# Performance work log

Measured on AMD Instinct MI355X. Metric: run time of the kernel, lower is better.

## Reference

```python
import jax, jax.numpy as jnp
import numpy as np

N_NODES = 100000

def _gcn_layer(h, src, dst, norm, W, b, n_nodes):
    # GCNConv: x @ W, then symmetric-normalized scatter-add over edges (incl. self-loops)
    h = h @ W                                  # [N, F_out]
    msg = h[src] * norm[:, None]               # [E_tot, F_out]
    out = jax.ops.segment_sum(msg, dst, num_segments=n_nodes)
    return out + b


def setup_inputs() -> dict:
    key = jax.random.key(0)
    k1, k2, k3, k4 = jax.random.split(key, 4)
    N, E, F_in, H, C = N_NODES, 3200000, 128, 16, 16
    x = jax.random.normal(k1, (N, F_in), dtype=jnp.float32)
    edge_index = jax.random.randint(k2, (2, E), 0, N, dtype=jnp.int64)
    W1 = jax.random.normal(k3, (F_in, H), dtype=jnp.float32) * (1.0 / np.sqrt(F_in))
    b1 = jnp.zeros((H,), dtype=jnp.float32)
    W2 = jax.random.normal(k4, (H, C), dtype=jnp.float32) * (1.0 / np.sqrt(H))
    b2 = jnp.zeros((C,), dtype=jnp.float32)
    return {"x": x, "edge_index": edge_index, "W1": W1, "b1": b1, "W2": W2, "b2": b2}


def reference(x, edge_index, W1, b1, W2, b2):
    N = x.shape[0]
    loops = jnp.arange(N, dtype=edge_index.dtype)
    src = jnp.concatenate([edge_index[0], loops])  # messages flow src -> dst (PyG convention)
    dst = jnp.concatenate([edge_index[1], loops])
    # symmetric normalization: deg^{-1/2}[src] * deg^{-1/2}[dst], deg counted on dst w/ self-loops
    deg = jnp.zeros((N,), dtype=x.dtype).at[dst].add(1.0)
    dinv = jax.lax.rsqrt(jnp.where(deg > 0, deg, 1.0))
    norm = dinv[src] * dinv[dst]                   # [E_tot]

    h = _gcn_layer(x, src, dst, norm, W1, b1, N)
    h = jax.nn.relu(h)
    # F.dropout(training=self.training): eval mode -> identity (deterministic reference)
    h = _gcn_layer(h, src, dst, norm, W2, b2, N)
    return jax.nn.log_softmax(h, axis=1)
```

## Files before the change

kernel.cpp:

```cpp
#include <hip/hip_runtime.h>
#include <hip/hip_bf16.h>
#include <math.h>


#define F_IN 128
#define H 16
#define NPB 128
#define MAX_NB 800
#define NBLK 256
#define BINT 1024
#define SMAX 4864
#define PFD 3

typedef __hip_bfloat16 bf16;

__device__ __forceinline__ float bflo(unsigned v) { return __uint_as_float(v << 16); }
__device__ __forceinline__ float bfhi(unsigned v) { return __uint_as_float(v & 0xffff0000u); }

__device__ __forceinline__ int swz(int p) { return (p & 7) * 32 + (p >> 3); }

__global__ void histA_kernel(const int* __restrict__ dst, int* __restrict__ hist_t,
                             int E, int NB) {
    __shared__ int h[MAX_NB];
    int b = swz(blockIdx.x);
    long long e0 = (long long)E * b / NBLK;
    long long e1 = (long long)E * (b + 1) / NBLK;
    for (int i = threadIdx.x; i < NB; i += BINT) h[i] = 0;
    __syncthreads();
    for (long long e = e0 + threadIdx.x; e < e1; e += BINT)
        atomicAdd(&h[dst[e] >> 7], 1);
    __syncthreads();
    for (int i = threadIdx.x; i < NB; i += BINT) hist_t[i * NBLK + b] = h[i];
}

__global__ void colscan_kernel(int* __restrict__ hist_t, int* __restrict__ btot) {
    __shared__ int s[NBLK];
    int j = blockIdx.x;
    int t = threadIdx.x;
    int v = hist_t[j * NBLK + t];
    s[t] = v;
    __syncthreads();
    for (int off = 1; off < NBLK; off <<= 1) {
        int w = (t >= off) ? s[t - off] : 0;
        __syncthreads();
        s[t] += w;
        __syncthreads();
    }
    hist_t[j * NBLK + t] = s[t] - v;
    if (t == NBLK - 1) btot[j] = s[t];
}

__global__ void bucketscan_kernel(const int* __restrict__ btot, int* __restrict__ base, int NB) {
    __shared__ int s[1024];
    int t = threadIdx.x;
    s[t] = (t < NB) ? btot[t] : 0;
    __syncthreads();
    for (int off = 1; off < 1024; off <<= 1) {
        int v = (t >= off) ? s[t - off] : 0;
        __syncthreads();
        s[t] += v;
        __syncthreads();
    }
    if (t < NB) base[t] = s[t] - btot[t];
    if (t == NB - 1) base[NB] = s[t];
}

__global__ void binC_kernel(const int* __restrict__ src, const int* __restrict__ dst,
                            const int* __restrict__ hist_t, const int* __restrict__ base,
                            unsigned* __restrict__ packed, int E, int NB) {
    __shared__ int pos[MAX_NB];
    int b = swz(blockIdx.x);
    long long e0 = (long long)E * b / NBLK;
    long long e1 = (long long)E * (b + 1) / NBLK;
    for (int i = threadIdx.x; i < NB; i += BINT)
        pos[i] = base[i] + hist_t[i * NBLK + b];
    __syncthreads();
    for (long long e = e0 + threadIdx.x; e < e1; e += BINT) {
        int d = dst[e];
        int bk = d >> 7;
        int p = atomicAdd(&pos[bk], 1);
        packed[p] = (unsigned)src[e] | ((unsigned)(d & 127) << 17);
    }
}

__global__ void sortcsr_kernel(const unsigned* __restrict__ packed, const int* __restrict__ base,
                               unsigned* __restrict__ sorted, int* __restrict__ rowptr,
                               float* __restrict__ dinv, int N, int E) {
    __shared__ unsigned ssort[SMAX];
    __shared__ int cnt[NPB], offs[NPB], cur[NPB];
    int b = blockIdx.x;
    int e0 = base[b];
    int len = base[b + 1] - e0;
    if (len > SMAX) len = SMAX;
    int T = blockDim.x;

    for (int i = threadIdx.x; i < NPB; i += T) cnt[i] = 0;
    __syncthreads();
    for (int i = threadIdx.x; i < len; i += T)
        atomicAdd(&cnt[packed[e0 + i] >> 17], 1);
    __syncthreads();
    if (threadIdx.x < NPB) offs[threadIdx.x] = cnt[threadIdx.x];
    __syncthreads();
    for (int off = 1; off < NPB; off <<= 1) {
        int v = 0;
        if (threadIdx.x < NPB && threadIdx.x >= off) v = offs[threadIdx.x - off];
        __syncthreads();
        if (threadIdx.x < NPB) offs[threadIdx.x] += v;
        __syncthreads();
    }
    if (threadIdx.x < NPB) {
        int ex = offs[threadIdx.x] - cnt[threadIdx.x];
        cur[threadIdx.x] = ex;
        int node = b * NPB + threadIdx.x;
        if (node < N) {
            rowptr[node] = e0 + ex;
            dinv[node] = rsqrtf(1.0f + (float)cnt[threadIdx.x]);
        }
    }
    __syncthreads();
    for (int i = threadIdx.x; i < len; i += T) {
        unsigned p = packed[e0 + i];
        int pos = atomicAdd(&cur[p >> 17], 1);
        ssort[pos] = p;
    }
    __syncthreads();
    for (int i = threadIdx.x; i < len; i += T) sorted[e0 + i] = ssort[i];
    if (b == 0 && threadIdx.x == 0) rowptr[N] = E;
}

#define XPAD 132
__global__ void xw1_kernel(const float* __restrict__ x, const float* __restrict__ W1,
                           const float* __restrict__ dinv, bf16* __restrict__ u, int n) {
    __shared__ float sW1[F_IN * H];
    __shared__ float sx[16 * XPAD];
    for (int t = threadIdx.x; t < F_IN * H; t += blockDim.x) sW1[t] = W1[t];

    int basei = blockIdx.x * 16;
    for (int idx = threadIdx.x; idx < 512; idx += 256) {
        int r = idx >> 5;
        int kk = (idx & 31) << 2;
        int row = basei + r;
        float4 v = make_float4(0.f, 0.f, 0.f, 0.f);
        if (row < n) v = *(const float4*)(x + (size_t)row * F_IN + kk);
        *(float4*)(sx + r * XPAD + kk) = v;
    }
    __syncthreads();

    int r = threadIdx.x >> 4;
    int j = threadIdx.x & 15;
    int row = basei + r;
    if (row >= n) return;

    const float* xr = sx + r * XPAD;
    float acc = 0.0f;
#pragma unroll 16
    for (int k = 0; k < F_IN; k++) acc += xr[k] * sW1[k * H + j];
    u[(size_t)row * H + j] = __float2bfloat16(dinv[row] * acc);
}

#define GATHER_TILE(UVPTR)                                                      \
    int lane = threadIdx.x & 63;                                                \
    int wave = threadIdx.x >> 6;                                                \
    int j4 = lane & 3, g = lane >> 2;                                           \
    int nodeBase = blockIdx.x * 64 + wave * 16;                                 \
    int r0c = 0, r1c = 0;                                                       \
    unsigned svc[PFD]; uint2 uvc[PFD];                                          \
    {   int node = nodeBase;                                                    \
        if (node < N) { r0c = rowptr[node]; r1c = rowptr[node + 1]; }           \
        _Pragma("unroll")                                                       \
        for (int m = 0; m < PFD; m++) {                                         \
            int k = r0c + g + 16 * m;                                           \
            if (k < r1c) svc[m] = sorted[k];                                    \
        }                                                                       \
        _Pragma("unroll")                                                       \
        for (int m = 0; m < PFD; m++) {                                         \
            int k = r0c + g + 16 * m;                                           \
            if (k < r1c) uvc[m] = UVPTR[(size_t)(svc[m] & 0x1FFFF) * 4 + j4];   \
        }                                                                       \
    }                                                                           \
    for (int t = 0; t < 16; t++) {                                              \
        int r0n = 0, r1n = 0;                                                   \
        unsigned svn[PFD];                                                      \
        if (t < 15) {                                                           \
            int nn = nodeBase + t + 1;                                          \
            if (nn < N) { r0n = rowptr[nn]; r1n = rowptr[nn + 1]; }             \
            _Pragma("unroll")                                                   \
            for (int m = 0; m < PFD; m++) {                                     \
                int k = r0n + g + 16 * m;                                       \
                if (k < r1n) svn[m] = sorted[k];                                \
            }                                                                   \
        }                                                                       \
        float ax = 0.f, ay = 0.f, az = 0.f, aw = 0.f;                           \
        _Pragma("unroll")                                                       \
        for (int m = 0; m < PFD; m++) {                                         \
            int k = r0c + g + 16 * m;                                           \
            if (k < r1c) {                                                      \
                ax += bflo(uvc[m].x); ay += bfhi(uvc[m].x);                     \
                az += bflo(uvc[m].y); aw += bfhi(uvc[m].y);                     \
            }                                                                   \
        }                                                                       \
        for (int k = r0c + g + 16 * PFD; k < r1c; k += 16) {                    \
            uint2 va = UVPTR[(size_t)(sorted[k] & 0x1FFFF) * 4 + j4];           \
            ax += bflo(va.x); ay += bfhi(va.x);                                 \
            az += bflo(va.y); aw += bfhi(va.y);                                 \
        }                                                                       \
        ax += __shfl_xor(ax, 4);  ay += __shfl_xor(ay, 4);                      \
        az += __shfl_xor(az, 4);  aw += __shfl_xor(aw, 4);                      \
        ax += __shfl_xor(ax, 8);  ay += __shfl_xor(ay, 8);                      \
        az += __shfl_xor(az, 8);  aw += __shfl_xor(aw, 8);                      \
        ax += __shfl_xor(ax, 16); ay += __shfl_xor(ay, 16);                     \
        az += __shfl_xor(az, 16); aw += __shfl_xor(aw, 16);                     \
        ax += __shfl_xor(ax, 32); ay += __shfl_xor(ay, 32);                     \
        az += __shfl_xor(az, 32); aw += __shfl_xor(aw, 32);                     \
        if (g == 0) {                                                           \
            float* tp = &tile[(wave * 16 + t) * 16 + 4 * j4];                   \
            tp[0] = ax; tp[1] = ay; tp[2] = az; tp[3] = aw;                     \
        }                                                                       \
        if (t < 15) {                                                           \
            r0c = r0n; r1c = r1n;                                               \
            _Pragma("unroll")                                                   \
            for (int m = 0; m < PFD; m++) {                                     \
                int k = r0n + g + 16 * m;                                       \
                svc[m] = svn[m];                                                \
                if (k < r1n) uvc[m] = UVPTR[(size_t)(svn[m] & 0x1FFFF) * 4 + j4]; \
            }                                                                   \
        }                                                                       \
    }

__global__ void gatherfin1_kernel(const unsigned* __restrict__ sorted, const int* __restrict__ rowptr,
                                  const bf16* __restrict__ u, const float* __restrict__ dinv,
                                  const float* __restrict__ b1, const float* __restrict__ W2,
                                  bf16* __restrict__ u2, int N) {
    __shared__ float tile[64 * 16];
    __shared__ float sW2[256];
    __shared__ float sb1[16];
    sW2[threadIdx.x] = W2[threadIdx.x];
    if (threadIdx.x < 16) sb1[threadIdx.x] = b1[threadIdx.x];

    const uint2* uvp = (const uint2*)u;
    GATHER_TILE(uvp)
    __syncthreads();

    int jj = threadIdx.x & 15;
    for (int rr = 0; rr < 4; rr++) {
        int rl = (threadIdx.x >> 4) + rr * 16;
        int node = blockIdx.x * 64 + rl;
        float h = 0.f, di = 0.f;
        if (node < N) {
            di = dinv[node];
            h = di * (tile[rl * 16 + jj] + __bfloat162float(u[(size_t)node * H + jj])) + sb1[jj];
            h = fmaxf(h, 0.f);
        }
        float acc2 = 0.f;
#pragma unroll
        for (int kk = 0; kk < 16; kk++) {
            float hk = __shfl(h, kk, 16);
            acc2 += hk * sW2[kk * 16 + jj];
        }
        if (node < N) u2[(size_t)node * H + jj] = __float2bfloat16(di * acc2);
    }
}

__global__ void gatherfin2_kernel(const unsigned* __restrict__ sorted, const int* __restrict__ rowptr,
                                  const bf16* __restrict__ u2, const float* __restrict__ dinv,
                                  const float* __restrict__ b2, float* __restrict__ out, int N) {
    __shared__ float tile[64 * 16];
    __shared__ float sb2[16];
    if (threadIdx.x < 16) sb2[threadIdx.x] = b2[threadIdx.x];

    const uint2* uvp = (const uint2*)u2;
    GATHER_TILE(uvp)
    __syncthreads();

    int jj = threadIdx.x & 15;
    for (int rr = 0; rr < 4; rr++) {
        int rl = (threadIdx.x >> 4) + rr * 16;
        int node = blockIdx.x * 64 + rl;
        if (node >= N) continue;
        float di = dinv[node];
        float v = di * (tile[rl * 16 + jj] + __bfloat162float(u2[(size_t)node * H + jj])) + sb2[jj];

        float m = v;
#pragma unroll
        for (int off = 8; off >= 1; off >>= 1) m = fmaxf(m, __shfl_xor(m, off, 16));
        float ex = __expf(v - m);
        float s = ex;
#pragma unroll
        for (int off = 8; off >= 1; off >>= 1) s += __shfl_xor(s, off, 16);

        out[(size_t)node * H + jj] = v - m - __logf(s);
    }
}

extern "C" void kernel_launch(void* const* d_in, const int* in_sizes, int n_in,
                              void* d_out, int out_size, void* d_ws, size_t ws_size,
                              hipStream_t stream) {
    const float* x = (const float*)d_in[0];
    const int* edge_index = (const int*)d_in[1];
    const float* W1 = (const float*)d_in[2];
    const float* b1 = (const float*)d_in[3];
    const float* W2 = (const float*)d_in[4];
    const float* b2 = (const float*)d_in[5];
    float* out = (float*)d_out;

    const int N = in_sizes[0] / F_IN;
    const int E = in_sizes[1] / 2;
    const int* src = edge_index;
    const int* dst = edge_index + E;
    const int NB = (N + NPB - 1) / NPB;

    float* dinv = (float*)d_ws;
    bf16* u = (bf16*)(dinv + N);
    bf16* u2 = (bf16*)((unsigned*)u + (size_t)N * H / 2);
    unsigned* packed = (unsigned*)((unsigned*)u2 + (size_t)N * H / 2);
    unsigned* sorted = packed + E;
    int* hist_t = (int*)(sorted + E);
    int* rowptr = hist_t + (size_t)MAX_NB * NBLK;
    int* btot = rowptr + N + 1;
    int* base = btot + NB;

    histA_kernel<<<NBLK, BINT, 0, stream>>>(dst, hist_t, E, NB);
    colscan_kernel<<<NB, NBLK, 0, stream>>>(hist_t, btot);
    bucketscan_kernel<<<1, 1024, 0, stream>>>(btot, base, NB);
    binC_kernel<<<NBLK, BINT, 0, stream>>>(src, dst, hist_t, base, packed, E, NB);
    sortcsr_kernel<<<NB, 512, 0, stream>>>(packed, base, sorted, rowptr, dinv, N, E);

    xw1_kernel<<<(N + 15) / 16, 256, 0, stream>>>(x, W1, dinv, u, N);
    gatherfin1_kernel<<<(N + 63) / 64, 256, 0, stream>>>(sorted, rowptr, u, dinv, b1, W2, u2, N);
    gatherfin2_kernel<<<(N + 63) / 64, 256, 0, stream>>>(sorted, rowptr, u2, dinv, b2, out, N);
}
```

Measured before the change: 234.6 us.

## Deepen gather prefetch pipeline and broadcast row pointers via wave shuffles

Each wave loads the 16 rowptr pairs once, one per lane, and hands them out with __shfl instead of reloading them for every node. The gather loop becomes a fully unrolled two-stage software pipeline: edge indices are prefetched two nodes ahead and feature rows one node ahead, using double-buffered registers. The aim is to hide more global-memory latency in the irregular gather, at the cost of more registers and possibly lower occupancy.

New measurement: 248.8 us. 1.06x slower.

```diff
diff --git a/kernel.cpp b/kernel.cpp
--- a/kernel.cpp
+++ b/kernel.cpp
@@ -163,43 +163,60 @@
     int wave = threadIdx.x >> 6;                                                \
     int j4 = lane & 3, g = lane >> 2;                                           \
     int nodeBase = blockIdx.x * 64 + wave * 16;                                 \
-    int r0c = 0, r1c = 0;                                                       \
-    unsigned svc[PFD]; uint2 uvc[PFD];                                          \
-    {   int node = nodeBase;                                                    \
-        if (node < N) { r0c = rowptr[node]; r1c = rowptr[node + 1]; }           \
+    int rA = 0, rB = 0;                                                         \
+    {   int nl = nodeBase + lane;                                               \
+        if (lane < 16 && nl < N) { rA = rowptr[nl]; rB = rowptr[nl + 1]; }      \
+    }                                                                           \
+    unsigned sv[2][PFD]; uint2 uv[2][PFD];                                      \
+    {                               \
+        int p00 = __shfl(rA, 0), p01 = __shfl(rB, 0);                           \
+        int p10 = __shfl(rA, 1), p11 = __shfl(rB, 1);                           \
         _Pragma("unroll")                                                       \
         for (int m = 0; m < PFD; m++) {                                         \
-            int k = r0c + g + 16 * m;                                           \
-            if (k < r1c) svc[m] = sorted[k];                                    \
+            int k = p00 + g + 16 * m;                                           \
+            if (k < p01) sv[0][m] = sorted[k];                                  \
         }                                                                       \
         _Pragma("unroll")                                                       \
         for (int m = 0; m < PFD; m++) {                                         \
-            int k = r0c + g + 16 * m;                                           \
-            if (k < r1c) uvc[m] = UVPTR[(size_t)(svc[m] & 0x1FFFF) * 4 + j4];   \
+            int k = p10 + g + 16 * m;                                           \
+            if (k < p11) sv[1][m] = sorted[k];                                  \
+        }                                                                       \
+        _Pragma("unroll")                                                       \
+        for (int m = 0; m < PFD; m++) {                                         \
+            int k = p00 + g + 16 * m;                                           \
+            if (k < p01) uv[0][m] = UVPTR[(size_t)(sv[0][m] & 0x1FFFF) * 4 + j4]; \
         }                                                                       \
     }                                                                           \
+    _Pragma("unroll")                                                           \
     for (int t = 0; t < 16; t++) {                                              \
-        int r0n = 0, r1n = 0;                                                   \
-        unsigned svn[PFD];                                                      \
-        if (t < 15) {                                                           \
-            int nn = nodeBase + t + 1;                                          \
-            if (nn < N) { r0n = rowptr[nn]; r1n = rowptr[nn + 1]; }             \
+        if (t + 2 < 16) {           \
+            int rn0 = __shfl(rA, t + 2), rn1 = __shfl(rB, t + 2);               \
             _Pragma("unroll")                                                   \
             for (int m = 0; m < PFD; m++) {                                     \
-                int k = r0n + g + 16 * m;                                       \
-                if (k < r1n) svn[m] = sorted[k];                                \
+                int k = rn0 + g + 16 * m;                                       \
+                if (k < rn1) sv[t & 1][m] = sorted[k];                          \
             }                                                                   \
         }                                                                       \
+        if (t + 1 < 16) {         \
+            int rn0 = __shfl(rA, t + 1), rn1 = __shfl(rB, t + 1);               \
+            _Pragma("unroll")                                                   \
+            for (int m = 0; m < PFD; m++) {                                     \
+                int k = rn0 + g + 16 * m;                                       \
+                if (k < rn1) uv[(t + 1) & 1][m] =                               \
+                    UVPTR[(size_t)(sv[(t + 1) & 1][m] & 0x1FFFF) * 4 + j4];     \
+            }                                                                   \
+        }                                                                       \
+        int rc0 = __shfl(rA, t), rc1 = __shfl(rB, t);                           \
         float ax = 0.f, ay = 0.f, az = 0.f, aw = 0.f;                           \
         _Pragma("unroll")                                                       \
         for (int m = 0; m < PFD; m++) {                                         \
-            int k = r0c + g + 16 * m;                                           \
-            if (k < r1c) {                                                      \
-                ax += bflo(uvc[m].x); ay += bfhi(uvc[m].x);                     \
-                az += bflo(uvc[m].y); aw += bfhi(uvc[m].y);                     \
+            int k = rc0 + g + 16 * m;                                           \
+            if (k < rc1) {                                                      \
+                ax += bflo(uv[t & 1][m].x); ay += bfhi(uv[t & 1][m].x);         \
+                az += bflo(uv[t & 1][m].y); aw += bfhi(uv[t & 1][m].y);         \
             }                                                                   \
         }                                                                       \
-        for (int k = r0c + g + 16 * PFD; k < r1c; k += 16) {                    \
+        for (int k = rc0 + g + 16 * PFD; k < rc1; k += 16) {                    \
             uint2 va = UVPTR[(size_t)(sorted[k] & 0x1FFFF) * 4 + j4];           \
             ax += bflo(va.x); ay += bfhi(va.x);                                 \
             az += bflo(va.y); aw += bfhi(va.y);                                 \
@@ -215,15 +232,6 @@
         if (g == 0) {                                                           \
             float* tp = &tile[(wave * 16 + t) * 16 + 4 * j4];                   \
             tp[0] = ax; tp[1] = ay; tp[2] = az; tp[3] = aw;                     \
-        }                                                                       \
-        if (t < 15) {                                                           \
-            r0c = r0n; r1c = r1n;                                               \
-            _Pragma("unroll")                                                   \
-            for (int m = 0; m < PFD; m++) {                                     \
-                int k = r0n + g + 16 * m;                                       \
-                svc[m] = svn[m];                                                \
-                if (k < r1n) uvc[m] = UVPTR[(size_t)(svn[m] & 0x1FFFF) * 4 + j4]; \
-            }                                                                   \
         }                                                                       \
     }
 
```
